# Kernel optimization log

Hardware: AMD Instinct MI355X
Metric: run time of the kernel (lower is better)

## Reference

```python
import jax, jax.numpy as jnp
import numpy as np

P, F_IN, HG, C, T, E, HOUT = 4096, 64, 64, 64, 32, 65536, 12
LEAKY_SLOPE = 0.2
LN_EPS = 1e-5


def setup_inputs() -> dict:
    key = jax.random.key(0)
    ks = jax.random.split(key, 14)
    g = lambda k, shape, scale: (jax.random.normal(k, shape, jnp.float32) * scale)
    return {
        "X": jax.random.normal(ks[0], (1, P, F_IN, T), jnp.float32),
        "edge_index": jax.random.randint(ks[1], (T, 2, E), 0, P, jnp.int32),
        # GATv2 params (single head)
        "Wl": g(ks[2], (F_IN, HG), 0.1),
        "Wr": g(ks[3], (F_IN, HG), 0.1),
        "att": g(ks[4], (HG,), 0.1),
        "gat_b": g(ks[5], (HG,), 0.02),
        # 1x1 time conv (HG -> C) and 1x1 residual conv (F_IN -> C)
        "W_time": g(ks[6], (C, HG), 0.1),
        "b_time": g(ks[7], (C,), 0.02),
        "W_res": g(ks[8], (C, F_IN), 0.1),
        "b_res": g(ks[9], (C,), 0.02),
        # LayerNorm over channel dim C
        "ln_g": jnp.ones((C,), jnp.float32),
        "ln_b": jnp.zeros((C,), jnp.float32),
        # final conv: Conv2d(in=T, out=HOUT, kernel=(1, C)) -> weight (HOUT, T, C)
        "W_final": g(ks[10], (HOUT, T, C), 0.05),
        "b_final": g(ks[11], (HOUT,), 0.02),
    }


def reference(X, edge_index, Wl, Wr, att, gat_b, W_time, b_time, W_res, b_res,
              ln_g, ln_b, W_final, b_final):
    Pn = X.shape[1]

    def gat_t(x, edges):
        # x: (P, F_IN), edges: (2, E) with edges[0]=src j, edges[1]=dst i
        src, dst = edges[0], edges[1]
        hl = x @ Wl                      # (P, HG) messages
        hr = x @ Wr                      # (P, HG) query side
        e = jax.nn.leaky_relu(hl[src] + hr[dst], LEAKY_SLOPE) @ att  # (E,)
        emax = jax.ops.segment_max(e, dst, num_segments=Pn)
        ex = jnp.exp(e - emax[dst])
        den = jax.ops.segment_sum(ex, dst, num_segments=Pn)
        alpha = ex / den[dst]            # softmax over in-edges of each dst
        return jax.ops.segment_sum(alpha[:, None] * hl[src], dst,
                                   num_segments=Pn) + gat_b  # (P, HG)

    xs = jnp.moveaxis(X[0], -1, 0)                     # (T, P, F_IN)
    X_hat = jax.nn.relu(jax.vmap(gat_t)(xs, edge_index))  # (T, P, HG)

    th = jnp.einsum('tph,ch->tpc', X_hat, W_time) + b_time  # time conv 1x1
    rs = jnp.einsum('tpf,cf->tpc', xs, W_res) + b_res       # residual conv 1x1
    y = jax.nn.relu(th + rs)                                 # (T, P, C)

    mu = jnp.mean(y, axis=-1, keepdims=True)
    var = jnp.var(y, axis=-1, keepdims=True)
    yn = (y - mu) * jax.lax.rsqrt(var + LN_EPS) * ln_g + ln_b  # (T, P, C)

    # final conv: in-channels = T, kernel (1, C) -> contract over t and c
    out = jnp.einsum('tpc,otc->po', yn, W_final) + b_final     # (P, HOUT)
    return out[None]                                           # (1, P, HOUT)
```

## Files before the change

kernel.cpp:

```cpp
#include <hip/hip_runtime.h>
#include <math.h>

#define NP 4096
#define F_IN 64
#define HG 64
#define NC 64
#define NT 32
#define NE 65536
#define HOUT 12
#define LEAKY 0.2f
#define LN_EPS 1e-5f

template <int CTRL>
__device__ __forceinline__ float dppadd(float v, float x) {
    int r = __builtin_amdgcn_update_dpp(0, __builtin_bit_cast(int, x), CTRL, 0xF, 0xF, false);
    return v + __builtin_bit_cast(float, r);
}
__device__ __forceinline__ float rowsum16(float v) {
    v = dppadd<0x128>(v, v);
    v = dppadd<0x124>(v, v);
    v = dppadd<0x122>(v, v);
    v = dppadd<0x121>(v, v);
    return v;
}
__device__ __forceinline__ float xrowsum(float v) {
    v = dppadd<0x142>(v, v);
    v = dppadd<0x143>(v, v);
    return v;
}
__device__ __forceinline__ float rdlane(float v, int l) {
    return __builtin_bit_cast(float, __builtin_amdgcn_readlane(__builtin_bit_cast(int, v), l));
}
__device__ __forceinline__ float wavered63(float v) {
    v = rowsum16(v);
    v = xrowsum(v);
    return rdlane(v, 63);
}
__device__ __forceinline__ float laneXorSum(float v) {
    v += __shfl_xor(v, 16, 64);
    v += __shfl_xor(v, 32, 64);
    return v;
}

#define FMA4(Acomp, B, r)                                                     \
    acc[r][0] += (Acomp) * (B).x; acc[r][1] += (Acomp) * (B).y;               \
    acc[r][2] += (Acomp) * (B).z; acc[r][3] += (Acomp) * (B).w;

__global__ __launch_bounds__(256) void k_prep(const float* __restrict__ W_time,
        const float* __restrict__ W_res,
        float* __restrict__ wtT, float* __restrict__ wrT) {
    int b = blockIdx.x, tid = threadIdx.x;
    if (b < 16) {
        int i = b * 256 + tid;
        wtT[i] = W_time[(i & 63) * 64 + (i >> 6)];
    } else {
        int i = (b - 16) * 256 + tid;
        wrT[i] = W_res[(i & 63) * 64 + (i >> 6)];
    }
}

__global__ __launch_bounds__(256) void k_hlhr(const float* __restrict__ X,
        const float* __restrict__ Wl, const float* __restrict__ Wr,
        const float* __restrict__ wrT, const float* __restrict__ b_res,
        float* __restrict__ hl, float* __restrict__ hr, float* __restrict__ rs) {
    __shared__ float xs[2][F_IN][36];
    __shared__ float bk[F_IN][132];
    int p0 = blockIdx.x * 2, tid = threadIdx.x;
    const float4* Xp = (const float4*)(X + (size_t)p0 * F_IN * NT);
    for (int i4 = tid; i4 < 1024; i4 += 256) {
        int pp = i4 >> 9, f = (i4 >> 3) & 63, t0 = (i4 & 7) * 4;
        *(float4*)&xs[pp][f][t0] = Xp[i4];
    }
    for (int i = tid; i < F_IN * HG; i += 256) {
        int f = i >> 6, h = i & 63;
        bk[f][h] = Wl[i];
        bk[f][64 + h] = Wr[i];
    }
    __syncthreads();
    {
        int ng = tid & 31, tg = tid >> 5;
        int n0 = ng * 4, col = (ng & 15) * 4, t0 = tg * 4;
        float acc[8][4];
#pragma unroll
        for (int i = 0; i < 8; ++i)
#pragma unroll
            for (int j = 0; j < 4; ++j) acc[i][j] = 0.f;
#pragma unroll 4
        for (int f = 0; f < F_IN; ++f) {
            float4 B = *(const float4*)&bk[f][n0];
            float4 A0 = *(const float4*)&xs[0][f][t0];
            float4 A1 = *(const float4*)&xs[1][f][t0];
            FMA4(A0.x, B, 0) FMA4(A0.y, B, 1) FMA4(A0.z, B, 2) FMA4(A0.w, B, 3)
            FMA4(A1.x, B, 4) FMA4(A1.y, B, 5) FMA4(A1.z, B, 6) FMA4(A1.w, B, 7)
        }
#pragma unroll
        for (int pp = 0; pp < 2; ++pp) {
#pragma unroll
            for (int i = 0; i < 4; ++i) {
                size_t rb = ((size_t)(t0 + i) * NP + p0 + pp) * HG;
                float4 v;
                v.x = acc[pp * 4 + i][0]; v.y = acc[pp * 4 + i][1];
                v.z = acc[pp * 4 + i][2]; v.w = acc[pp * 4 + i][3];
                if (ng < 16) *(float4*)&hl[rb + col] = v;
                else         *(float4*)&hr[rb + col] = v;
            }
        }
    }
    __syncthreads();
    for (int i = tid; i < F_IN * NC; i += 256) bk[i >> 6][i & 63] = wrT[i];
    __syncthreads();
    {
        int cg = tid & 15, tg = tid >> 4;
        int c0 = cg * 4, t0 = tg * 2;
        float4 br4 = *(const float4*)&b_res[c0];
        float acc[4][4];
#pragma unroll
        for (int i = 0; i < 4; ++i) {
            acc[i][0] = br4.x; acc[i][1] = br4.y; acc[i][2] = br4.z; acc[i][3] = br4.w;
        }
#pragma unroll 4
        for (int f = 0; f < F_IN; ++f) {
            float4 B = *(const float4*)&bk[f][c0];
            float2 A0 = *(const float2*)&xs[0][f][t0];
            float2 A1 = *(const float2*)&xs[1][f][t0];
            FMA4(A0.x, B, 0) FMA4(A0.y, B, 1)
            FMA4(A1.x, B, 2) FMA4(A1.y, B, 3)
        }
#pragma unroll
        for (int pp = 0; pp < 2; ++pp) {
#pragma unroll
            for (int i = 0; i < 2; ++i) {
                float4 v;
                v.x = acc[pp * 2 + i][0]; v.y = acc[pp * 2 + i][1];
                v.z = acc[pp * 2 + i][2]; v.w = acc[pp * 2 + i][3];
                *(float4*)&rs[((size_t)(t0 + i) * NP + p0 + pp) * NC + c0] = v;
            }
        }
    }
}


__global__ __launch_bounds__(256) void k_count(const int* __restrict__ EI,
                                               int* __restrict__ cnt2) {
    __shared__ int loc[1024];
    int b = blockIdx.x;
    int j = b >> 3;
    int t = (b & 7) + 8 * (j & 3);
    int cr = j >> 2;
    int c = cr & 3, r = cr >> 2;
    int tid = threadIdx.x;
    loc[tid] = 0; loc[tid + 256] = 0; loc[tid + 512] = 0; loc[tid + 768] = 0;
    __syncthreads();
    int base = r << 10;
    const int4* dstA = (const int4*)(EI + (size_t)t * 2 * NE + NE) + c * (NE / 16);
    for (int i = tid; i < NE / 16; i += 256) {
        int4 d = dstA[i];
        if ((d.x >> 10) == r) atomicAdd(&loc[d.x - base], 1);
        if ((d.y >> 10) == r) atomicAdd(&loc[d.y - base], 1);
        if ((d.z >> 10) == r) atomicAdd(&loc[d.z - base], 1);
        if ((d.w >> 10) == r) atomicAdd(&loc[d.w - base], 1);
    }
    __syncthreads();
    int o = (t * 4 + c) * NP + base + tid;
    cnt2[o] = loc[tid];
    cnt2[o + 256] = loc[tid + 256];
    cnt2[o + 512] = loc[tid + 512];
    cnt2[o + 768] = loc[tid + 768];
}

__global__ __launch_bounds__(256) void k_scan(const int* __restrict__ cnt2,
        int* __restrict__ cnt, int* __restrict__ start, int* __restrict__ start2) {
    __shared__ int ctot[256];
    int t = blockIdx.x, tid = threadIdx.x;
    int vals[16];
    int s = 0;
    int dbase = tid * 16;
#pragma unroll
    for (int k = 0; k < 16; ++k) {
        int d = dbase + k;
        int deg = cnt2[(t * 4 + 0) * NP + d] + cnt2[(t * 4 + 1) * NP + d]
                + cnt2[(t * 4 + 2) * NP + d] + cnt2[(t * 4 + 3) * NP + d];
        cnt[t * NP + d] = deg;
        vals[k] = s; s += deg;
    }
    ctot[tid] = s;
    __syncthreads();
    int inc = s;
    for (int dd = 1; dd < 256; dd <<= 1) {
        int v = (tid >= dd) ? ctot[tid - dd] : 0;
        __syncthreads();
        ctot[tid] += v;
        __syncthreads();
    }
    int exc = ctot[tid] - inc;
#pragma unroll
    for (int k = 0; k < 16; ++k) {
        int d = dbase + k;
        int st = t * NE + exc + vals[k];
        start[t * NP + d] = st;
        int q0 = cnt2[(t * 4 + 0) * NP + d];
        int q1 = cnt2[(t * 4 + 1) * NP + d];
        int q2 = cnt2[(t * 4 + 2) * NP + d];
        start2[(t * 4 + 0) * NP + d] = st; st += q0;
        start2[(t * 4 + 1) * NP + d] = st; st += q1;
        start2[(t * 4 + 2) * NP + d] = st; st += q2;
        start2[(t * 4 + 3) * NP + d] = st;
    }
}

__global__ __launch_bounds__(256) void k_fill(const int* __restrict__ EI,
        const int* __restrict__ start2, int* __restrict__ ssrc) {
    __shared__ int curs_l[1024];
    int b = blockIdx.x;
    int j = b >> 3;
    int t = (b & 7) + 8 * (j & 3);
    int cr = j >> 2;
    int c = cr & 3, r = cr >> 2;
    int tid = threadIdx.x;
    int base = r << 10;
    int o = (t * 4 + c) * NP + base + tid;
    curs_l[tid] = start2[o];
    curs_l[tid + 256] = start2[o + 256];
    curs_l[tid + 512] = start2[o + 512];
    curs_l[tid + 768] = start2[o + 768];
    __syncthreads();
    const int4* srcA = (const int4*)(EI + (size_t)t * 2 * NE) + c * (NE / 16);
    const int4* dstA = (const int4*)(EI + (size_t)t * 2 * NE + NE) + c * (NE / 16);
    for (int i = tid; i < NE / 16; i += 256) {
        int4 s = srcA[i];
        int4 d = dstA[i];
        if ((d.x >> 10) == r) { int sl = atomicAdd(&curs_l[d.x - base], 1); ssrc[sl] = s.x; }
        if ((d.y >> 10) == r) { int sl = atomicAdd(&curs_l[d.y - base], 1); ssrc[sl] = s.y; }
        if ((d.z >> 10) == r) { int sl = atomicAdd(&curs_l[d.z - base], 1); ssrc[sl] = s.z; }
        if ((d.w >> 10) == r) { int sl = atomicAdd(&curs_l[d.w - base], 1); ssrc[sl] = s.w; }
    }
}

__global__ __launch_bounds__(256) void k_gat(const float* __restrict__ hl,
        float* __restrict__ hr,
        const int* __restrict__ start, const int* __restrict__ cnt,
        const int* __restrict__ ssrc,
        const float* __restrict__ att, const float* __restrict__ gat_b) {
    __shared__ int sidx[4][64];
    int b = blockIdx.x;
    int k = b >> 3;
    int t = (b & 7) + 8 * (k >> 10);
    int ws = threadIdx.x >> 6;
    int i = (k & 1023) * 4 + ws;
    int lane = threadIdx.x & 63;
    int row = lane >> 4;
    int c0 = (lane & 15) * 4;
    size_t nbase = ((size_t)t * NP + i) * HG;
    const float* hlt = hl + (size_t)t * NP * HG;
    float4 r4 = *(const float4*)&hr[nbase + c0];
    float4 at4 = *(const float4*)&att[c0];
    int s0 = start[t * NP + i];
    int deg = cnt[t * NP + i];
    float l = 0.f;
    float4 acc = {0.f, 0.f, 0.f, 0.f};
    for (int base = 0; base < deg; base += 64) {
        int chunk = deg - base;
        chunk = (chunk < 64) ? chunk : 64;
        int stage = (lane < chunk) ? lane : 0;
        sidx[ws][lane] = ssrc[s0 + base + stage];
        int nfull = chunk & ~7;
        int j = 0;
        for (; j < nfull; j += 8) {
            int src0 = sidx[ws][j + row];
            int src1 = sidx[ws][j + 4 + row];
            float4 h0 = *(const float4*)&hlt[((size_t)src0 << 6) + c0];
            float4 h1 = *(const float4*)&hlt[((size_t)src1 << 6) + c0];
            float4 z0, z1;
            z0.x = h0.x + r4.x; z0.y = h0.y + r4.y; z0.z = h0.z + r4.z; z0.w = h0.w + r4.w;
            z1.x = h1.x + r4.x; z1.y = h1.y + r4.y; z1.z = h1.z + r4.z; z1.w = h1.w + r4.w;
            z0.x = fmaxf(z0.x, LEAKY * z0.x); z0.y = fmaxf(z0.y, LEAKY * z0.y);
            z0.z = fmaxf(z0.z, LEAKY * z0.z); z0.w = fmaxf(z0.w, LEAKY * z0.w);
            z1.x = fmaxf(z1.x, LEAKY * z1.x); z1.y = fmaxf(z1.y, LEAKY * z1.y);
            z1.z = fmaxf(z1.z, LEAKY * z1.z); z1.w = fmaxf(z1.w, LEAKY * z1.w);
            float e0 = rowsum16(z0.x * at4.x + z0.y * at4.y + z0.z * at4.z + z0.w * at4.w);
            float e1 = rowsum16(z1.x * at4.x + z1.y * at4.y + z1.z * at4.z + z1.w * at4.w);
            float w0 = __expf(e0);
            float w1 = __expf(e1);
            l += w0 + w1;
            acc.x += w0 * h0.x + w1 * h1.x;
            acc.y += w0 * h0.y + w1 * h1.y;
            acc.z += w0 * h0.z + w1 * h1.z;
            acc.w += w0 * h0.w + w1 * h1.w;
        }
        for (; j < chunk; j += 4) {
            int jj = j + row;
            int src = sidx[ws][(jj < chunk) ? jj : 0];
            float4 ha = *(const float4*)&hlt[((size_t)src << 6) + c0];
            float4 za;
            za.x = ha.x + r4.x; za.y = ha.y + r4.y; za.z = ha.z + r4.z; za.w = ha.w + r4.w;
            za.x = fmaxf(za.x, LEAKY * za.x);
            za.y = fmaxf(za.y, LEAKY * za.y);
            za.z = fmaxf(za.z, LEAKY * za.z);
            za.w = fmaxf(za.w, LEAKY * za.w);
            float ep = za.x * at4.x + za.y * at4.y + za.z * at4.z + za.w * at4.w;
            float e = rowsum16(ep);
            float w = __expf(e);
            w = (jj < chunk) ? w : 0.f;
            l += w;
            acc.x += w * ha.x; acc.y += w * ha.y; acc.z += w * ha.z; acc.w += w * ha.w;
        }
    }
    float lt = laneXorSum(l);
    acc.x = laneXorSum(acc.x);
    acc.y = laneXorSum(acc.y);
    acc.z = laneXorSum(acc.z);
    acc.w = laneXorSum(acc.w);
    if (row == 0) {
        float inv = (deg > 0) ? (1.0f / lt) : 0.f;
        float4 gb = *(const float4*)&gat_b[c0];
        float4 o;
        o.x = fmaxf(acc.x * inv + gb.x, 0.f);
        o.y = fmaxf(acc.y * inv + gb.y, 0.f);
        o.z = fmaxf(acc.z * inv + gb.z, 0.f);
        o.w = fmaxf(acc.w * inv + gb.w, 0.f);
        *(float4*)&hr[nbase + c0] = o;
    }
}

__global__ __launch_bounds__(256) void k_post(const float* __restrict__ Xhat,
        const float* __restrict__ wtT, const float* __restrict__ b_time,
        const float* __restrict__ rs, const float* __restrict__ ln_g,
        const float* __restrict__ ln_b, float* __restrict__ yn) {
    __shared__ float in_t[64][68];
    __shared__ float bk[64][68];
    int bx = blockIdx.x;
    int t = bx >> 6;
    int p0 = (bx & 63) * 64;
    int tid = threadIdx.x;
    const float4* src = (const float4*)(Xhat + ((size_t)t * NP + p0) * HG);
    for (int i4 = tid; i4 < 1024; i4 += 256) {
        int pp = i4 >> 4, c4 = (i4 & 15) * 4;
        *(float4*)&in_t[pp][c4] = src[i4];
    }
    const float4* wsrc = (const float4*)wtT;
    for (int i4 = tid; i4 < 1024; i4 += 256) {
        int h = i4 >> 4, c4 = (i4 & 15) * 4;
        *(float4*)&bk[h][c4] = wsrc[i4];
    }
    __syncthreads();
    int cg = tid & 15, pg = tid >> 4;
    int c0 = cg * 4, pl = pg * 4;
    float4 bt4 = *(const float4*)&b_time[c0];
    float acc[4][4];
#pragma unroll
    for (int i = 0; i < 4; ++i) {
        acc[i][0] = bt4.x; acc[i][1] = bt4.y; acc[i][2] = bt4.z; acc[i][3] = bt4.w;
    }
#pragma unroll
    for (int k4 = 0; k4 < 16; ++k4) {
        float4 A0 = *(const float4*)&in_t[pl + 0][k4 * 4];
        float4 A1 = *(const float4*)&in_t[pl + 1][k4 * 4];
        float4 A2 = *(const float4*)&in_t[pl + 2][k4 * 4];
        float4 A3 = *(const float4*)&in_t[pl + 3][k4 * 4];
        float4 B0 = *(const float4*)&bk[k4 * 4 + 0][c0];
        FMA4(A0.x, B0, 0) FMA4(A1.x, B0, 1) FMA4(A2.x, B0, 2) FMA4(A3.x, B0, 3)
        float4 B1 = *(const float4*)&bk[k4 * 4 + 1][c0];
        FMA4(A0.y, B1, 0) FMA4(A1.y, B1, 1) FMA4(A2.y, B1, 2) FMA4(A3.y, B1, 3)
        float4 B2 = *(const float4*)&bk[k4 * 4 + 2][c0];
        FMA4(A0.z, B2, 0) FMA4(A1.z, B2, 1) FMA4(A2.z, B2, 2) FMA4(A3.z, B2, 3)
        float4 B3 = *(const float4*)&bk[k4 * 4 + 3][c0];
        FMA4(A0.w, B3, 0) FMA4(A1.w, B3, 1) FMA4(A2.w, B3, 2) FMA4(A3.w, B3, 3)
    }
    float4 lg = *(const float4*)&ln_g[c0];
    float4 lb = *(const float4*)&ln_b[c0];
#pragma unroll
    for (int i = 0; i < 4; ++i) {
        size_t prow = (size_t)t * NP + p0 + pl + i;
        float4 r4 = *(const float4*)&rs[prow * NC + c0];
        float y0 = fmaxf(acc[i][0] + r4.x, 0.f), y1 = fmaxf(acc[i][1] + r4.y, 0.f);
        float y2 = fmaxf(acc[i][2] + r4.z, 0.f), y3 = fmaxf(acc[i][3] + r4.w, 0.f);
        float s = rowsum16(y0 + y1 + y2 + y3);
        float ss = rowsum16(y0 * y0 + y1 * y1 + y2 * y2 + y3 * y3);
        float mu = s * (1.f / 64.f);
        float var = ss * (1.f / 64.f) - mu * mu;
        float rsd = rsqrtf(var + LN_EPS);
        float4 o;
        o.x = (y0 - mu) * rsd * lg.x + lb.x;
        o.y = (y1 - mu) * rsd * lg.y + lb.y;
        o.z = (y2 - mu) * rsd * lg.z + lb.z;
        o.w = (y3 - mu) * rsd * lg.w + lb.w;
        *(float4*)&yn[prow * NC + c0] = o;
    }
}

__global__ __launch_bounds__(256) void k_final(const float* __restrict__ yn,
        const float* __restrict__ Wf, const float* __restrict__ bf,
        float* __restrict__ out) {
    int p = blockIdx.x * 4 + (threadIdx.x >> 6);
    int lane = threadIdx.x & 63;
    float acc[HOUT];
#pragma unroll
    for (int o = 0; o < HOUT; ++o) acc[o] = 0.f;
    for (int k = 0; k < NT; ++k) {
        float yv = yn[((size_t)k * NP + p) * NC + lane];
#pragma unroll
        for (int o = 0; o < HOUT; ++o)
            acc[o] += yv * Wf[(size_t)o * NT * NC + k * NC + lane];
    }
#pragma unroll
    for (int o = 0; o < HOUT; ++o) {
        float s = wavered63(acc[o]);
        if (lane == 0) out[p * HOUT + o] = s + bf[o];
    }
}

extern "C" void kernel_launch(void* const* d_in, const int* in_sizes, int n_in,
                              void* d_out, int out_size, void* d_ws, size_t ws_size,
                              hipStream_t stream) {
    const float* X      = (const float*)d_in[0];
    const int*   EI     = (const int*)d_in[1];
    const float* Wl     = (const float*)d_in[2];
    const float* Wr     = (const float*)d_in[3];
    const float* att    = (const float*)d_in[4];
    const float* gat_b  = (const float*)d_in[5];
    const float* W_time = (const float*)d_in[6];
    const float* b_time = (const float*)d_in[7];
    const float* W_res  = (const float*)d_in[8];
    const float* b_res  = (const float*)d_in[9];
    const float* ln_g   = (const float*)d_in[10];
    const float* ln_b   = (const float*)d_in[11];
    const float* Wf     = (const float*)d_in[12];
    const float* bf     = (const float*)d_in[13];
    float* out = (float*)d_out;

    char* ws = (char*)d_ws;
    const size_t MB = 1024 * 1024;
    float* hl    = (float*)(ws);
    float* hr    = (float*)(ws + 32 * MB);
    float* rs    = (float*)(ws + 64 * MB);
    int*   ssrc  = (int*)  (ws + 96 * MB);
    int*   cnt   = (int*)  (ws + 104 * MB);
    int*   strt  = (int*)  (ws + 104 * MB + 512 * 1024);
    float* wtT   = (float*)(ws + 105 * MB);
    float* wrT   = (float*)(ws + 105 * MB + 16384);
    int*   cnt2  = (int*)  (ws + 106 * MB);
    int*   strt2 = (int*)  (ws + 108 * MB);
    float* yn    = hl;

    k_prep <<<32, 256, 0, stream>>>(W_time, W_res, wtT, wrT);
    k_hlhr <<<NP / 2, 256, 0, stream>>>(X, Wl, Wr, wrT, b_res, hl, hr, rs);
    k_count<<<512, 256, 0, stream>>>(EI, cnt2);
    k_scan <<<NT, 256, 0, stream>>>(cnt2, cnt, strt, strt2);
    k_fill <<<512, 256, 0, stream>>>(EI, strt2, ssrc);
    k_gat  <<<(NT * NP) / 4, 256, 0, stream>>>(hl, hr, strt, cnt, ssrc, att, gat_b);
    k_post <<<NT * (NP / 64), 256, 0, stream>>>(hr, wtT, b_time, rs, ln_g, ln_b, yn);
    k_final<<<NP / 4, 256, 0, stream>>>(yn, Wf, bf, out);
}
```

Baseline: 290.6 us.

## Parallelize CSR scan across segments using per-wave partial sums from count kernel

```diff
diff --git a/kernel.cpp b/kernel.cpp
--- a/kernel.cpp
+++ b/kernel.cpp
@@ -39,6 +39,11 @@
 __device__ __forceinline__ float laneXorSum(float v) {
     v += __shfl_xor(v, 16, 64);
     v += __shfl_xor(v, 32, 64);
+    return v;
+}
+__device__ __forceinline__ int waveSumInt(int v) {
+#pragma unroll
+    for (int d = 1; d < 64; d <<= 1) v += __shfl_xor(v, d, 64);
     return v;
 }
 
@@ -139,9 +144,8 @@
     }
 }
 
-
 __global__ __launch_bounds__(256) void k_count(const int* __restrict__ EI,
-                                               int* __restrict__ cnt2) {
+        int* __restrict__ cnt2, int* __restrict__ segsum2) {
     __shared__ int loc[1024];
     int b = blockIdx.x;
     int j = b >> 3;
@@ -166,46 +170,50 @@
     cnt2[o + 256] = loc[tid + 256];
     cnt2[o + 512] = loc[tid + 512];
     cnt2[o + 768] = loc[tid + 768];
+    int wv = tid >> 6, lane = tid & 63;
+    int s = loc[wv * 256 + lane] + loc[wv * 256 + lane + 64]
+          + loc[wv * 256 + lane + 128] + loc[wv * 256 + lane + 192];
+    s = waveSumInt(s);
+    if (lane == 0) segsum2[(t * 4 + c) * 16 + r * 4 + wv] = s;
 }
 
 __global__ __launch_bounds__(256) void k_scan(const int* __restrict__ cnt2,
-        int* __restrict__ cnt, int* __restrict__ start, int* __restrict__ start2) {
-    __shared__ int ctot[256];
-    int t = blockIdx.x, tid = threadIdx.x;
-    int vals[16];
-    int s = 0;
-    int dbase = tid * 16;
-#pragma unroll
-    for (int k = 0; k < 16; ++k) {
-        int d = dbase + k;
-        int deg = cnt2[(t * 4 + 0) * NP + d] + cnt2[(t * 4 + 1) * NP + d]
-                + cnt2[(t * 4 + 2) * NP + d] + cnt2[(t * 4 + 3) * NP + d];
-        cnt[t * NP + d] = deg;
-        vals[k] = s; s += deg;
-    }
-    ctot[tid] = s;
-    __syncthreads();
-    int inc = s;
+        const int* __restrict__ segsum2, int* __restrict__ cnt,
+        int* __restrict__ start, int* __restrict__ start2) {
+    __shared__ int sc[256];
+    __shared__ int preS;
+    int b = blockIdx.x;
+    int t = b >> 4, seg = b & 15;
+    int tid = threadIdx.x;
+    if (tid < 64) {
+        int c = tid >> 4, s = tid & 15;
+        int v = (s < seg) ? segsum2[(t * 4 + c) * 16 + s] : 0;
+        v = waveSumInt(v);
+        if (tid == 0) preS = v;
+    }
+    int d = seg * 256 + tid;
+    int q0 = cnt2[(t * 4 + 0) * NP + d];
+    int q1 = cnt2[(t * 4 + 1) * NP + d];
+    int q2 = cnt2[(t * 4 + 2) * NP + d];
+    int q3 = cnt2[(t * 4 + 3) * NP + d];
+    int deg = q0 + q1 + q2 + q3;
+    sc[tid] = deg;
+    __syncthreads();
+    int pre = preS;
     for (int dd = 1; dd < 256; dd <<= 1) {
-        int v = (tid >= dd) ? ctot[tid - dd] : 0;
+        int v = (tid >= dd) ? sc[tid - dd] : 0;
         __syncthreads();
-        ctot[tid] += v;
+        sc[tid] += v;
         __syncthreads();
     }
-    int exc = ctot[tid] - inc;
-#pragma unroll
-    for (int k = 0; k < 16; ++k) {
-        int d = dbase + k;
-        int st = t * NE + exc + vals[k];
-        start[t * NP + d] = st;
-        int q0 = cnt2[(t * 4 + 0) * NP + d];
-        int q1 = cnt2[(t * 4 + 1) * NP + d];
-        int q2 = cnt2[(t * 4 + 2) * NP + d];
-        start2[(t * 4 + 0) * NP + d] = st; st += q0;
-        start2[(t * 4 + 1) * NP + d] = st; st += q1;
-        start2[(t * 4 + 2) * NP + d] = st; st += q2;
-        start2[(t * 4 + 3) * NP + d] = st;
-    }
+    int exc = sc[tid] - deg;
+    int st = t * NE + pre + exc;
+    cnt[t * NP + d] = deg;
+    start[t * NP + d] = st;
+    start2[(t * 4 + 0) * NP + d] = st; st += q0;
+    start2[(t * 4 + 1) * NP + d] = st; st += q1;
+    start2[(t * 4 + 2) * NP + d] = st; st += q2;
+    start2[(t * 4 + 3) * NP + d] = st;
 }
 
 __global__ __launch_bounds__(256) void k_fill(const int* __restrict__ EI,
@@ -329,8 +337,9 @@
     __shared__ float in_t[64][68];
     __shared__ float bk[64][68];
     int bx = blockIdx.x;
-    int t = bx >> 6;
-    int p0 = (bx & 63) * 64;
+    int j = bx >> 3;
+    int t = (bx & 7) + 8 * (j & 3);
+    int p0 = (j >> 2) * 64;
     int tid = threadIdx.x;
     const float4* src = (const float4*)(Xhat + ((size_t)t * NP + p0) * HG);
     for (int i4 = tid; i4 < 1024; i4 += 256) {
@@ -438,14 +447,15 @@
     int*   strt  = (int*)  (ws + 104 * MB + 512 * 1024);
     float* wtT   = (float*)(ws + 105 * MB);
     float* wrT   = (float*)(ws + 105 * MB + 16384);
+    int*   segs2 = (int*)  (ws + 105 * MB + 32768);
     int*   cnt2  = (int*)  (ws + 106 * MB);
     int*   strt2 = (int*)  (ws + 108 * MB);
     float* yn    = hl;
 
     k_prep <<<32, 256, 0, stream>>>(W_time, W_res, wtT, wrT);
     k_hlhr <<<NP / 2, 256, 0, stream>>>(X, Wl, Wr, wrT, b_res, hl, hr, rs);
-    k_count<<<512, 256, 0, stream>>>(EI, cnt2);
-    k_scan <<<NT, 256, 0, stream>>>(cnt2, cnt, strt, strt2);
+    k_count<<<512, 256, 0, stream>>>(EI, cnt2, segs2);
+    k_scan <<<NT * 16, 256, 0, stream>>>(cnt2, segs2, cnt, strt, strt2);
     k_fill <<<512, 256, 0, stream>>>(EI, strt2, ssrc);
     k_gat  <<<(NT * NP) / 4, 256, 0, stream>>>(hl, hr, strt, cnt, ssrc, att, gat_b);
     k_post <<<NT * (NP / 64), 256, 0, stream>>>(hr, wtT, b_time, rs, ln_g, ln_b, yn);
```

New measurement: 284.0 us. -2.3%, faster.
